# Kernel optimization log

Hardware: AMD Instinct MI355X
Metric: run time of the kernel (lower is better)

Reference implementation:

```python
import jax, jax.numpy as jnp
import numpy as np

D_MODEL = 1024
NUM_HEADS = 16
HEAD_DIM = D_MODEL // NUM_HEADS  # 64
# NOTE: the original module passes scale=attention_head_size, so scores are
# MULTIPLIED by head_dim (64), not divided by sqrt(head_dim). Faithful quirk.
SCALE = float(HEAD_DIM)


def setup_inputs() -> dict:
    key = jax.random.key(0)
    ks = jax.random.split(key, 6)
    bs, s, d = 2, 2048, D_MODEL
    q = jax.random.normal(ks[0], (bs, s, d), dtype=jnp.float32)
    k = jax.random.normal(ks[1], (bs, s, d), dtype=jnp.float32)
    v = jax.random.normal(ks[2], (bs, s, d), dtype=jnp.float32)
    # nn.Linear weights, shape (out, in); no bias (qkv_bias=False)
    init = 1.0 / np.sqrt(d)
    Wq = jax.random.uniform(ks[3], (d, d), jnp.float32, -init, init)
    Wk = jax.random.uniform(ks[4], (d, d), jnp.float32, -init, init)
    Wv = jax.random.uniform(ks[5], (d, d), jnp.float32, -init, init)
    return {"q": q, "k": k, "v": v, "Wq": Wq, "Wk": Wk, "Wv": Wv}


def _split_heads(x):
    bs, s, _ = x.shape
    return x.reshape(bs, s, NUM_HEADS, HEAD_DIM).transpose(0, 2, 1, 3)  # bhsd


def reference(q, k, v, Wq, Wk, Wv):
    bs, s, d = q.shape
    qh = _split_heads(q @ Wq.T)  # [b,h,s,hd]
    kh = _split_heads(k @ Wk.T)
    vh = _split_heads(v @ Wv.T)
    sims = jnp.einsum('bhqd,bhkd->bhqk', qh, kh) * SCALE
    attn = jax.nn.softmax(sims, axis=-1)
    out = jnp.einsum('bhqk,bhkd->bhqd', attn, vh)  # [b,h,s,hd]
    out = out.transpose(0, 2, 1, 3).reshape(bs, s, d)
    return out
```

## Files before the change

### kernel.cpp

```cpp
#include <hip/hip_runtime.h>


typedef _Float16 half4 __attribute__((ext_vector_type(4)));
typedef _Float16 half8 __attribute__((ext_vector_type(8)));
typedef float floatx4 __attribute__((ext_vector_type(4)));

#define MFMA_F16(a, b, c) __builtin_amdgcn_mfma_f32_16x16x32_f16((a), (b), (c), 0, 0, 0)

constexpr int SEQ = 2048;
constexpr int DM = 1024;
constexpr int NH = 16;
constexpr int HD = 64;
constexpr float QSCALE = 92.33248261689366f;

__device__ __forceinline__ void gl2lds16(const _Float16* g, _Float16* l) {
  __builtin_amdgcn_global_load_lds(
      (const __attribute__((address_space(1))) void*)g,
      (__attribute__((address_space(3))) void*)l, 16, 0, 0);
}

__device__ inline void split4(const float4 f, half4& h, half4& l) {
  h[0] = (_Float16)f.x; l[0] = (_Float16)(f.x - (float)h[0]);
  h[1] = (_Float16)f.y; l[1] = (_Float16)(f.y - (float)h[1]);
  h[2] = (_Float16)f.z; l[2] = (_Float16)(f.z - (float)h[2]);
  h[3] = (_Float16)f.w; l[3] = (_Float16)(f.w - (float)h[3]);
}

__global__ __launch_bounds__(256) void convert_kernel(
    const float* __restrict__ x, const float* __restrict__ W,
    _Float16* __restrict__ xh, _Float16* __restrict__ xl,
    _Float16* __restrict__ Wh, _Float16* __restrict__ Wl, int do_lo)
{
  if (blockIdx.x < 4096) {
    int idx = blockIdx.x * 256 + threadIdx.x;
    float4 f = ((const float4*)x)[idx];
    half4 h, l; split4(f, h, l);
    *(half4*)(xh + (size_t)idx * 4) = h;
    if (do_lo) *(half4*)(xl + (size_t)idx * 4) = l;
  } else {
    int idx = (blockIdx.x - 4096) * 256 + threadIdx.x;
    float4 f = ((const float4*)W)[idx];
    half4 h, l; split4(f, h, l);
    *(half4*)(Wh + (size_t)idx * 4) = h;
    if (do_lo) *(half4*)(Wl + (size_t)idx * 4) = l;
  }
}

__global__ __launch_bounds__(256, 1) void proj_kernel(
    const _Float16* __restrict__ Ahg, const _Float16* __restrict__ Alg,
    const _Float16* __restrict__ Bhg, const _Float16* __restrict__ Blg,
    _Float16* __restrict__ yh, _Float16* __restrict__ yl,
    float scale, int three)
{
  __shared__ __align__(16) _Float16 Ahs[128][64];
  __shared__ __align__(16) _Float16 Als[128][64];
  __shared__ __align__(16) _Float16 Bhs[128][64];
  __shared__ __align__(16) _Float16 Bls[128][64];

  const int tid = threadIdx.x;
  const int bm = blockIdx.x;
  const int bn = blockIdx.y;
  const int lane = tid & 63, l15 = lane & 15, quad = lane >> 4;
  const int w = tid >> 6, wm = w >> 1, wn = w & 1;

  const int r8 = lane >> 3;
  const int cp8 = (((lane & 7) ^ r8)) * 8;
  int grow[4]; _Float16* la[4]; _Float16* lal[4]; _Float16* lb[4]; _Float16* lbl[4];
  #pragma unroll
  for (int i = 0; i < 4; i++) {
    const int g = w * 4 + i;
    grow[i] = g * 8 + r8;
    la[i]  = &Ahs[0][0] + g * 512;
    lal[i] = &Als[0][0] + g * 512;
    lb[i]  = &Bhs[0][0] + g * 512;
    lbl[i] = &Bls[0][0] + g * 512;
  }

  floatx4 acc[4][4];
  #pragma unroll
  for (int mt = 0; mt < 4; mt++)
    #pragma unroll
    for (int nt = 0; nt < 4; nt++)
      acc[mt][nt] = (floatx4){0.f, 0.f, 0.f, 0.f};

  for (int kk = 0; kk < DM; kk += 64) {
    __syncthreads();
    #pragma unroll
    for (int i = 0; i < 4; i++) {
      const size_t ga = (size_t)(bm * 128 + grow[i]) * DM + kk + cp8;
      const size_t gb = (size_t)(bn * 128 + grow[i]) * DM + kk + cp8;
      gl2lds16(Ahg + ga, la[i]);
      gl2lds16(Bhg + gb, lb[i]);
      if (three) {
        gl2lds16(Alg + ga, lal[i]);
        gl2lds16(Blg + gb, lbl[i]);
      }
    }
    __syncthreads();

    #pragma unroll
    for (int kc = 0; kc < 2; kc++) {
      const int swz = ((kc * 4 + quad) ^ (l15 & 7)) * 8;
      half8 ah[4], bh_[4], al[4], bl[4];
      #pragma unroll
      for (int t = 0; t < 4; t++) {
        ah[t]  = *(const half8*)&Ahs[wm * 64 + t * 16 + l15][swz];
        bh_[t] = *(const half8*)&Bhs[wn * 64 + t * 16 + l15][swz];
        if (three) {
          al[t] = *(const half8*)&Als[wm * 64 + t * 16 + l15][swz];
          bl[t] = *(const half8*)&Bls[wn * 64 + t * 16 + l15][swz];
        }
      }
      if (three) {
        #pragma unroll
        for (int mt = 0; mt < 4; mt++)
          #pragma unroll
          for (int nt = 0; nt < 4; nt++) {
            floatx4 t0 = MFMA_F16(ah[mt], bh_[nt], acc[mt][nt]);
            t0 = MFMA_F16(ah[mt], bl[nt], t0);
            acc[mt][nt] = MFMA_F16(al[mt], bh_[nt], t0);
          }
      } else {
        #pragma unroll
        for (int mt = 0; mt < 4; mt++)
          #pragma unroll
          for (int nt = 0; nt < 4; nt++)
            acc[mt][nt] = MFMA_F16(ah[mt], bh_[nt], acc[mt][nt]);
      }
    }
  }

  #pragma unroll
  for (int mt = 0; mt < 4; mt++)
    #pragma unroll
    for (int nt = 0; nt < 4; nt++)
      #pragma unroll
      for (int r = 0; r < 4; r++) {
        int gm = bm * 128 + wm * 64 + mt * 16 + quad * 4 + r;
        int gn = bn * 128 + wn * 64 + nt * 16 + l15;
        int b = gm >> 11, s = gm & 2047;
        int h = gn >> 6, d = gn & 63;
        size_t idx = ((size_t)(b * NH + h) * SEQ + s) * HD + d;
        float val = acc[mt][nt][r] * scale;
        _Float16 hi = (_Float16)val;
        yh[idx] = hi;
        if (three) yl[idx] = (_Float16)(val - (float)hi);
      }
}

__global__ __launch_bounds__(256) void transpose_v(const _Float16* __restrict__ vh,
                                                   _Float16* __restrict__ vhT)
{
  __shared__ __align__(16) _Float16 T[128][72];
  const int bh = blockIdx.x, sc = blockIdx.y, tid = threadIdx.x;
  const _Float16* src = vh + ((size_t)bh * SEQ + sc * 128) * HD;
  #pragma unroll
  for (int i = 0; i < 4; i++) {
    int c = i * 256 + tid, row = c >> 3, off = (c & 7) * 8;
    *(half8*)&T[row][off] = *(const half8*)(src + (size_t)row * HD + off);
  }
  __syncthreads();
  _Float16* dst = vhT + (size_t)bh * HD * SEQ + sc * 128;
  #pragma unroll
  for (int i = 0; i < 4; i++) {
    int c = i * 256 + tid, hd = c >> 4, off = (c & 15) * 8;
    int base32 = off & ~31, qsel = (off >> 3) & 3;
    half8 vv;
    #pragma unroll
    for (int j = 0; j < 8; j++) {
      int s_local = base32 + 16 * (j >> 2) + 4 * qsel + (j & 3);
      vv[j] = T[s_local][hd];
    }
    *(half8*)(dst + (size_t)hd * SEQ + off) = vv;
  }
}

__global__ __launch_bounds__(256, 4) void flash_kernel(
    const _Float16* __restrict__ qh_hi, const _Float16* __restrict__ qh_lo,
    const _Float16* __restrict__ kh_hi, const _Float16* __restrict__ kh_lo,
    const _Float16* __restrict__ vhT, float* __restrict__ Op, float2* __restrict__ ml)
{
  __shared__ __align__(16) _Float16 Kh[64][64];
  __shared__ __align__(16) _Float16 Kl[64][64];
  __shared__ __align__(16) _Float16 Vt[64][64];

  const int id = blockIdx.x;
  const int seq_ = id >> 3;
  const int bh = (id & 7) + 8 * (seq_ & 3);
  const int rem = seq_ >> 2;
  const int qb = rem & 15;
  const int kh = rem >> 4;
  const int tid = threadIdx.x;
  const int wq = tid >> 6;
  const int lane = tid & 63, l15 = lane & 15, quad = lane >> 4;

  const size_t bh_off = (size_t)bh * SEQ * HD;
  const _Float16* __restrict__ kh_p = kh_hi + bh_off;
  const _Float16* __restrict__ kl_p = kh_lo + bh_off;
  const _Float16* __restrict__ vt_p = vhT + (size_t)bh * HD * SEQ;
  const int qrow0 = qb * 128 + wq * 32;

  half8 bqh[2][2], bql[2][2];
  #pragma unroll
  for (int g = 0; g < 2; g++) {
    const _Float16* qp_h = qh_hi + bh_off + (size_t)(qrow0 + g * 16 + l15) * HD;
    const _Float16* qp_l = qh_lo + bh_off + (size_t)(qrow0 + g * 16 + l15) * HD;
    #pragma unroll
    for (int kc = 0; kc < 2; kc++) {
      bqh[g][kc] = *(const half8*)(qp_h + kc * 32 + quad * 8);
      bql[g][kc] = *(const half8*)(qp_l + kc * 32 + quad * 8);
    }
  }

  const int r8 = lane >> 3;
  const int cp8 = ((lane & 7) ^ r8) * 8;

  float m_[2] = {-3.0e38f, -3.0e38f};
  float l_[2] = {0.f, 0.f};
  floatx4 Oacc[2][4];
  #pragma unroll
  for (int g = 0; g < 2; g++)
    #pragma unroll
    for (int nd = 0; nd < 4; nd++) Oacc[g][nd] = (floatx4){0.f, 0.f, 0.f, 0.f};

  const int kt0 = kh * 16;
  for (int kt = kt0; kt < kt0 + 16; kt++) {
    const int kbase = kt * 64;
    __syncthreads();
    #pragma unroll
    for (int i = 0; i < 2; i++) {
      const int g = wq * 2 + i;
      const int r = g * 8 + r8;
      gl2lds16(kh_p + (size_t)(kbase + r) * HD + cp8, &Kh[0][0] + g * 512);
      gl2lds16(kl_p + (size_t)(kbase + r) * HD + cp8, &Kl[0][0] + g * 512);
      gl2lds16(vt_p + (size_t)r * SEQ + kbase + cp8, &Vt[0][0] + g * 512);
    }
    __syncthreads();

    floatx4 sacc[2][4];
    #pragma unroll
    for (int nt = 0; nt < 4; nt++) {
      const int r7 = l15 & 7;
      half8 akh0 = *(const half8*)&Kh[nt * 16 + l15][((0 * 4 + quad) ^ r7) * 8];
      half8 akh1 = *(const half8*)&Kh[nt * 16 + l15][((1 * 4 + quad) ^ r7) * 8];
      half8 akl0 = *(const half8*)&Kl[nt * 16 + l15][((0 * 4 + quad) ^ r7) * 8];
      half8 akl1 = *(const half8*)&Kl[nt * 16 + l15][((1 * 4 + quad) ^ r7) * 8];
      #pragma unroll
      for (int g = 0; g < 2; g++) {
        floatx4 s4 = (floatx4){0.f, 0.f, 0.f, 0.f};
        s4 = MFMA_F16(akh0, bqh[g][0], s4);
        s4 = MFMA_F16(akh1, bqh[g][1], s4);
        s4 = MFMA_F16(akh0, bql[g][0], s4);
        s4 = MFMA_F16(akh1, bql[g][1], s4);
        s4 = MFMA_F16(akl0, bqh[g][0], s4);
        s4 = MFMA_F16(akl1, bqh[g][1], s4);
        sacc[g][nt] = s4;
      }
    }

    half8 av[4][2];
    {
      const int r7 = l15 & 7;
      #pragma unroll
      for (int nd = 0; nd < 4; nd++) {
        av[nd][0] = *(const half8*)&Vt[nd * 16 + l15][((0 * 4 + quad) ^ r7) * 8];
        av[nd][1] = *(const half8*)&Vt[nd * 16 + l15][((1 * 4 + quad) ^ r7) * 8];
      }
    }

    #pragma unroll
    for (int g = 0; g < 2; g++) {
      float rmax = sacc[g][0][0];
      #pragma unroll
      for (int nt = 0; nt < 4; nt++)
        #pragma unroll
        for (int r = 0; r < 4; r++) rmax = fmaxf(rmax, sacc[g][nt][r]);
      rmax = fmaxf(rmax, __shfl_xor(rmax, 16, 64));
      rmax = fmaxf(rmax, __shfl_xor(rmax, 32, 64));
      const float mnew = fmaxf(m_[g], rmax);
      const float alpha = exp2f(m_[g] - mnew);
      m_[g] = mnew;

      float rsum = 0.f;
      #pragma unroll
      for (int nt = 0; nt < 4; nt++)
        #pragma unroll
        for (int r = 0; r < 4; r++) {
          float p = exp2f(sacc[g][nt][r] - mnew);
          sacc[g][nt][r] = p;
          rsum += p;
        }
      rsum += __shfl_xor(rsum, 16, 64);
      rsum += __shfl_xor(rsum, 32, 64);
      l_[g] = l_[g] * alpha + rsum;

      half8 bp8[2];
      #pragma unroll
      for (int kc = 0; kc < 2; kc++)
        #pragma unroll
        for (int j = 0; j < 8; j++)
          bp8[kc][j] = (_Float16)sacc[g][2 * kc + (j >> 2)][j & 3];

      #pragma unroll
      for (int nd = 0; nd < 4; nd++) {
        Oacc[g][nd][0] *= alpha; Oacc[g][nd][1] *= alpha;
        Oacc[g][nd][2] *= alpha; Oacc[g][nd][3] *= alpha;
        Oacc[g][nd] = MFMA_F16(av[nd][0], bp8[0], Oacc[g][nd]);
        Oacc[g][nd] = MFMA_F16(av[nd][1], bp8[1], Oacc[g][nd]);
      }
    }
  }

  const size_t fqbase = (size_t)bh * SEQ + qrow0;
  #pragma unroll
  for (int g = 0; g < 2; g++) {
    const size_t fq = fqbase + g * 16 + l15;
    float* ob = Op + ((size_t)kh * 65536 + fq) * HD;
    #pragma unroll
    for (int nd = 0; nd < 4; nd++) {
      float4 vv;
      vv.x = Oacc[g][nd][0]; vv.y = Oacc[g][nd][1];
      vv.z = Oacc[g][nd][2]; vv.w = Oacc[g][nd][3];
      *(float4*)(ob + nd * 16 + quad * 4) = vv;
    }
    if (quad == 0) ml[kh * 65536 + fq] = make_float2(m_[g], l_[g]);
  }
}

__global__ __launch_bounds__(256) void merge_kernel(const float* __restrict__ Op,
                                                    const float2* __restrict__ ml,
                                                    float* __restrict__ out)
{
  const int tid = threadIdx.x;
  const int fq = blockIdx.x * 64 + (tid >> 2);
  const int dp = (tid & 3) * 16;
  float2 m0 = ml[fq], m1 = ml[65536 + fq];
  float M = fmaxf(m0.x, m1.x);
  float w0 = exp2f(m0.x - M), w1 = exp2f(m1.x - M);
  float rinv = 1.0f / (m0.y * w0 + m1.y * w1);
  int bh = fq >> 11, s = fq & 2047, b = bh >> 4, h = bh & 15;
  float* ob = out + ((size_t)(b * SEQ + s)) * DM + h * HD + dp;
  const float* p0 = Op + (size_t)fq * HD + dp;
  const float* p1 = p0 + (size_t)65536 * HD;
  #pragma unroll
  for (int j = 0; j < 4; j++) {
    float4 a = *(const float4*)(p0 + 4 * j);
    float4 c = *(const float4*)(p1 + 4 * j);
    float4 r;
    r.x = (a.x * w0 + c.x * w1) * rinv;
    r.y = (a.y * w0 + c.y * w1) * rinv;
    r.z = (a.z * w0 + c.z * w1) * rinv;
    r.w = (a.w * w0 + c.w * w1) * rinv;
    *(float4*)(ob + 4 * j) = r;
  }
}

extern "C" void kernel_launch(void* const* d_in, const int* in_sizes, int n_in,
                              void* d_out, int out_size, void* d_ws, size_t ws_size,
                              hipStream_t stream) {
  const float* q  = (const float*)d_in[0];
  const float* k  = (const float*)d_in[1];
  const float* v  = (const float*)d_in[2];
  const float* Wq = (const float*)d_in[3];
  const float* Wk = (const float*)d_in[4];
  const float* Wv = (const float*)d_in[5];
  float* out = (float*)d_out;

  char* W = (char*)d_ws;
  const size_t MiB = 1ull << 20;
  _Float16* qh_hi = (_Float16*)(W + 0 * MiB);
  _Float16* qh_lo = (_Float16*)(W + 8 * MiB);
  _Float16* kh_hi = (_Float16*)(W + 16 * MiB);
  _Float16* kh_lo = (_Float16*)(W + 24 * MiB);
  _Float16* vhT   = (_Float16*)(W + 32 * MiB);
  _Float16* vh    = (_Float16*)(W + 40 * MiB);
  _Float16* xh    = (_Float16*)(W + 48 * MiB);
  _Float16* xl    = (_Float16*)(W + 56 * MiB);
  _Float16* Wh    = (_Float16*)(W + 64 * MiB);
  _Float16* Wl    = (_Float16*)(W + 66 * MiB);
  float*    Op    = (float*)  (W + 40 * MiB);
  float2*   mlp   = (float2*) (W + 72 * MiB);

  convert_kernel<<<5120, 256, 0, stream>>>(q, Wq, xh, xl, Wh, Wl, 1);
  proj_kernel<<<dim3(32, 8), 256, 0, stream>>>(xh, xl, Wh, Wl, qh_hi, qh_lo, QSCALE, 1);
  convert_kernel<<<5120, 256, 0, stream>>>(k, Wk, xh, xl, Wh, Wl, 1);
  proj_kernel<<<dim3(32, 8), 256, 0, stream>>>(xh, xl, Wh, Wl, kh_hi, kh_lo, 1.0f, 1);
  convert_kernel<<<5120, 256, 0, stream>>>(v, Wv, xh, xl, Wh, Wl, 0);
  proj_kernel<<<dim3(32, 8), 256, 0, stream>>>(xh, xl, Wh, Wl, vh, vh, 1.0f, 0);

  transpose_v<<<dim3(32, 16), 256, 0, stream>>>(vh, vhT);
  flash_kernel<<<1024, 256, 0, stream>>>(qh_hi, qh_lo, kh_hi, kh_lo, vhT, Op, mlp);
  merge_kernel<<<1024, 256, 0, stream>>>(Op, mlp, out);
}
```

Baseline: 319.7 us.

## Shrink projection M-tile to 64 and register-prefetch next K/V tile in flash kernel

The projection GEMM tile shrinks from 128x128 to 64x128, doubling the grid to 512 blocks and allowing two blocks per CU. The aim is better occupancy and load balance across the GPU's many CUs. The flash kernel now loads the next K/V tile from global memory into registers while computing on the current tile, then writes it to LDS after a barrier, overlapping memory latency with compute. This costs extra registers and an extra barrier per iteration. The projection change also adds B-tile reloads per output element.

```diff
diff --git a/kernel.cpp b/kernel.cpp
--- a/kernel.cpp
+++ b/kernel.cpp
@@ -46,14 +46,14 @@
   }
 }
 
-__global__ __launch_bounds__(256, 1) void proj_kernel(
+__global__ __launch_bounds__(256, 2) void proj_kernel(
     const _Float16* __restrict__ Ahg, const _Float16* __restrict__ Alg,
     const _Float16* __restrict__ Bhg, const _Float16* __restrict__ Blg,
     _Float16* __restrict__ yh, _Float16* __restrict__ yl,
     float scale, int three)
 {
-  __shared__ __align__(16) _Float16 Ahs[128][64];
-  __shared__ __align__(16) _Float16 Als[128][64];
+  __shared__ __align__(16) _Float16 Ahs[64][64];
+  __shared__ __align__(16) _Float16 Als[64][64];
   __shared__ __align__(16) _Float16 Bhs[128][64];
   __shared__ __align__(16) _Float16 Bls[128][64];
 
@@ -64,21 +64,11 @@
   const int w = tid >> 6, wm = w >> 1, wn = w & 1;
 
   const int r8 = lane >> 3;
-  const int cp8 = (((lane & 7) ^ r8)) * 8;
-  int grow[4]; _Float16* la[4]; _Float16* lal[4]; _Float16* lb[4]; _Float16* lbl[4];
-  #pragma unroll
-  for (int i = 0; i < 4; i++) {
-    const int g = w * 4 + i;
-    grow[i] = g * 8 + r8;
-    la[i]  = &Ahs[0][0] + g * 512;
-    lal[i] = &Als[0][0] + g * 512;
-    lb[i]  = &Bhs[0][0] + g * 512;
-    lbl[i] = &Bls[0][0] + g * 512;
-  }
-
-  floatx4 acc[4][4];
-  #pragma unroll
-  for (int mt = 0; mt < 4; mt++)
+  const int cp8 = ((lane & 7) ^ r8) * 8;
+
+  floatx4 acc[2][4];
+  #pragma unroll
+  for (int mt = 0; mt < 2; mt++)
     #pragma unroll
     for (int nt = 0; nt < 4; nt++)
       acc[mt][nt] = (floatx4){0.f, 0.f, 0.f, 0.f};
@@ -86,34 +76,38 @@
   for (int kk = 0; kk < DM; kk += 64) {
     __syncthreads();
     #pragma unroll
+    for (int i = 0; i < 2; i++) {
+      const int g = w * 2 + i;
+      const size_t ga = (size_t)(bm * 64 + g * 8 + r8) * DM + kk + cp8;
+      gl2lds16(Ahg + ga, &Ahs[0][0] + g * 512);
+      if (three) gl2lds16(Alg + ga, &Als[0][0] + g * 512);
+    }
+    #pragma unroll
     for (int i = 0; i < 4; i++) {
-      const size_t ga = (size_t)(bm * 128 + grow[i]) * DM + kk + cp8;
-      const size_t gb = (size_t)(bn * 128 + grow[i]) * DM + kk + cp8;
-      gl2lds16(Ahg + ga, la[i]);
-      gl2lds16(Bhg + gb, lb[i]);
-      if (three) {
-        gl2lds16(Alg + ga, lal[i]);
-        gl2lds16(Blg + gb, lbl[i]);
-      }
+      const int g = w * 4 + i;
+      const size_t gb = (size_t)(bn * 128 + g * 8 + r8) * DM + kk + cp8;
+      gl2lds16(Bhg + gb, &Bhs[0][0] + g * 512);
+      if (three) gl2lds16(Blg + gb, &Bls[0][0] + g * 512);
     }
     __syncthreads();
 
     #pragma unroll
     for (int kc = 0; kc < 2; kc++) {
       const int swz = ((kc * 4 + quad) ^ (l15 & 7)) * 8;
-      half8 ah[4], bh_[4], al[4], bl[4];
-      #pragma unroll
-      for (int t = 0; t < 4; t++) {
-        ah[t]  = *(const half8*)&Ahs[wm * 64 + t * 16 + l15][swz];
-        bh_[t] = *(const half8*)&Bhs[wn * 64 + t * 16 + l15][swz];
-        if (three) {
-          al[t] = *(const half8*)&Als[wm * 64 + t * 16 + l15][swz];
-          bl[t] = *(const half8*)&Bls[wn * 64 + t * 16 + l15][swz];
-        }
+      half8 ah[2], al[2], bh_[4], bl[4];
+      #pragma unroll
+      for (int mt = 0; mt < 2; mt++) {
+        ah[mt] = *(const half8*)&Ahs[wm * 32 + mt * 16 + l15][swz];
+        if (three) al[mt] = *(const half8*)&Als[wm * 32 + mt * 16 + l15][swz];
+      }
+      #pragma unroll
+      for (int nt = 0; nt < 4; nt++) {
+        bh_[nt] = *(const half8*)&Bhs[wn * 64 + nt * 16 + l15][swz];
+        if (three) bl[nt] = *(const half8*)&Bls[wn * 64 + nt * 16 + l15][swz];
       }
       if (three) {
         #pragma unroll
-        for (int mt = 0; mt < 4; mt++)
+        for (int mt = 0; mt < 2; mt++)
           #pragma unroll
           for (int nt = 0; nt < 4; nt++) {
             floatx4 t0 = MFMA_F16(ah[mt], bh_[nt], acc[mt][nt]);
@@ -122,7 +116,7 @@
           }
       } else {
         #pragma unroll
-        for (int mt = 0; mt < 4; mt++)
+        for (int mt = 0; mt < 2; mt++)
           #pragma unroll
           for (int nt = 0; nt < 4; nt++)
             acc[mt][nt] = MFMA_F16(ah[mt], bh_[nt], acc[mt][nt]);
@@ -131,12 +125,12 @@
   }
 
   #pragma unroll
-  for (int mt = 0; mt < 4; mt++)
+  for (int mt = 0; mt < 2; mt++)
     #pragma unroll
     for (int nt = 0; nt < 4; nt++)
       #pragma unroll
       for (int r = 0; r < 4; r++) {
-        int gm = bm * 128 + wm * 64 + mt * 16 + quad * 4 + r;
+        int gm = bm * 64 + wm * 32 + mt * 16 + quad * 4 + r;
         int gn = bn * 128 + wn * 64 + nt * 16 + l15;
         int b = gm >> 11, s = gm & 2047;
         int h = gn >> 6, d = gn & 63;
@@ -224,9 +218,8 @@
     for (int nd = 0; nd < 4; nd++) Oacc[g][nd] = (floatx4){0.f, 0.f, 0.f, 0.f};
 
   const int kt0 = kh * 16;
-  for (int kt = kt0; kt < kt0 + 16; kt++) {
-    const int kbase = kt * 64;
-    __syncthreads();
+  {
+    const int kbase = kt0 * 64;
     #pragma unroll
     for (int i = 0; i < 2; i++) {
       const int g = wq * 2 + i;
@@ -235,7 +228,24 @@
       gl2lds16(kl_p + (size_t)(kbase + r) * HD + cp8, &Kl[0][0] + g * 512);
       gl2lds16(vt_p + (size_t)r * SEQ + kbase + cp8, &Vt[0][0] + g * 512);
     }
+  }
+
+  for (int kt = kt0; kt < kt0 + 16; kt++) {
     __syncthreads();
+
+    const bool hasnext = (kt + 1 < kt0 + 16);
+    half8 rkh[2], rkl[2], rvt[2];
+    if (hasnext) {
+      const int kb2 = (kt + 1) * 64;
+      #pragma unroll
+      for (int i = 0; i < 2; i++) {
+        const int g = wq * 2 + i;
+        const int r = g * 8 + r8;
+        rkh[i] = *(const half8*)(kh_p + (size_t)(kb2 + r) * HD + cp8);
+        rkl[i] = *(const half8*)(kl_p + (size_t)(kb2 + r) * HD + cp8);
+        rvt[i] = *(const half8*)(vt_p + (size_t)r * SEQ + kb2 + cp8);
+      }
+    }
 
     floatx4 sacc[2][4];
     #pragma unroll
@@ -307,6 +317,17 @@
         Oacc[g][nd][2] *= alpha; Oacc[g][nd][3] *= alpha;
         Oacc[g][nd] = MFMA_F16(av[nd][0], bp8[0], Oacc[g][nd]);
         Oacc[g][nd] = MFMA_F16(av[nd][1], bp8[1], Oacc[g][nd]);
+      }
+    }
+
+    __syncthreads();
+    if (hasnext) {
+      #pragma unroll
+      for (int i = 0; i < 2; i++) {
+        const int g = wq * 2 + i;
+        *(half8*)(&Kh[0][0] + g * 512 + lane * 8) = rkh[i];
+        *(half8*)(&Kl[0][0] + g * 512 + lane * 8) = rkl[i];
+        *(half8*)(&Vt[0][0] + g * 512 + lane * 8) = rvt[i];
       }
     }
   }
@@ -382,11 +403,11 @@
   float2*   mlp   = (float2*) (W + 72 * MiB);
 
   convert_kernel<<<5120, 256, 0, stream>>>(q, Wq, xh, xl, Wh, Wl, 1);
-  proj_kernel<<<dim3(32, 8), 256, 0, stream>>>(xh, xl, Wh, Wl, qh_hi, qh_lo, QSCALE, 1);
+  proj_kernel<<<dim3(64, 8), 256, 0, stream>>>(xh, xl, Wh, Wl, qh_hi, qh_lo, QSCALE, 1);
   convert_kernel<<<5120, 256, 0, stream>>>(k, Wk, xh, xl, Wh, Wl, 1);
-  proj_kernel<<<dim3(32, 8), 256, 0, stream>>>(xh, xl, Wh, Wl, kh_hi, kh_lo, 1.0f, 1);
+  proj_kernel<<<dim3(64, 8), 256, 0, stream>>>(xh, xl, Wh, Wl, kh_hi, kh_lo, 1.0f, 1);
   convert_kernel<<<5120, 256, 0, stream>>>(v, Wv, xh, xl, Wh, Wl, 0);
-  proj_kernel<<<dim3(32, 8), 256, 0, stream>>>(xh, xl, Wh, Wl, vh, vh, 1.0f, 0);
+  proj_kernel<<<dim3(64, 8), 256, 0, stream>>>(xh, xl, Wh, Wl, vh, vh, 1.0f, 0);
 
   transpose_v<<<dim3(32, 16), 256, 0, stream>>>(vh, vhT);
   flash_kernel<<<1024, 256, 0, stream>>>(qh_hi, qh_lo, kh_hi, kh_lo, vhT, Op, mlp);
```

New measurement: 518.6 us. 62.2% more time.

## Split KV range four ways and load V fragments directly from global

Applied to the files above, without the earlier changes.

The flash kernel is templated on the number of KV splits. When the workspace allows, it launches 2048 blocks with a 4-way KV split and a matching generalized merge kernel, which doubles grid parallelism. V tiles no longer go through LDS; each lane reads its half8 V fragments straight from the pre-transposed global buffer, which removes one LDS buffer and its async copies. The tradeoff is more partial-output traffic in the merge and uncoalesced, uncached-in-LDS global V reads. The block-index decoding also changes, which may break whichever bh/qb mapping the previous ordering intended.

```diff
diff --git a/kernel.cpp b/kernel.cpp
--- a/kernel.cpp
+++ b/kernel.cpp
@@ -175,6 +175,7 @@
   }
 }
 
+template<int KSPLIT>
 __global__ __launch_bounds__(256, 4) void flash_kernel(
     const _Float16* __restrict__ qh_hi, const _Float16* __restrict__ qh_lo,
     const _Float16* __restrict__ kh_hi, const _Float16* __restrict__ kh_lo,
@@ -182,12 +183,11 @@
 {
   __shared__ __align__(16) _Float16 Kh[64][64];
   __shared__ __align__(16) _Float16 Kl[64][64];
-  __shared__ __align__(16) _Float16 Vt[64][64];
-
+
+  constexpr int NKT = 32 / KSPLIT;
   const int id = blockIdx.x;
-  const int seq_ = id >> 3;
-  const int bh = (id & 7) + 8 * (seq_ & 3);
-  const int rem = seq_ >> 2;
+  const int bh = (id & 7) + 8 * ((id >> 3) & 3);
+  const int rem = id >> 5;
   const int qb = rem & 15;
   const int kh = rem >> 4;
   const int tid = threadIdx.x;
@@ -223,8 +223,8 @@
     #pragma unroll
     for (int nd = 0; nd < 4; nd++) Oacc[g][nd] = (floatx4){0.f, 0.f, 0.f, 0.f};
 
-  const int kt0 = kh * 16;
-  for (int kt = kt0; kt < kt0 + 16; kt++) {
+  const int kt0 = kh * NKT;
+  for (int kt = kt0; kt < kt0 + NKT; kt++) {
     const int kbase = kt * 64;
     __syncthreads();
     #pragma unroll
@@ -233,7 +233,6 @@
       const int r = g * 8 + r8;
       gl2lds16(kh_p + (size_t)(kbase + r) * HD + cp8, &Kh[0][0] + g * 512);
       gl2lds16(kl_p + (size_t)(kbase + r) * HD + cp8, &Kl[0][0] + g * 512);
-      gl2lds16(vt_p + (size_t)r * SEQ + kbase + cp8, &Vt[0][0] + g * 512);
     }
     __syncthreads();
 
@@ -259,13 +258,11 @@
     }
 
     half8 av[4][2];
-    {
-      const int r7 = l15 & 7;
-      #pragma unroll
-      for (int nd = 0; nd < 4; nd++) {
-        av[nd][0] = *(const half8*)&Vt[nd * 16 + l15][((0 * 4 + quad) ^ r7) * 8];
-        av[nd][1] = *(const half8*)&Vt[nd * 16 + l15][((1 * 4 + quad) ^ r7) * 8];
-      }
+    #pragma unroll
+    for (int nd = 0; nd < 4; nd++) {
+      const _Float16* vp = vt_p + (size_t)(nd * 16 + l15) * SEQ + kbase;
+      av[nd][0] = *(const half8*)(vp + quad * 8);
+      av[nd][1] = *(const half8*)(vp + 32 + quad * 8);
     }
 
     #pragma unroll
@@ -327,6 +324,7 @@
   }
 }
 
+template<int KSPLIT>
 __global__ __launch_bounds__(256) void merge_kernel(const float* __restrict__ Op,
                                                     const float2* __restrict__ ml,
                                                     float* __restrict__ out)
@@ -334,23 +332,33 @@
   const int tid = threadIdx.x;
   const int fq = blockIdx.x * 64 + (tid >> 2);
   const int dp = (tid & 3) * 16;
-  float2 m0 = ml[fq], m1 = ml[65536 + fq];
-  float M = fmaxf(m0.x, m1.x);
-  float w0 = exp2f(m0.x - M), w1 = exp2f(m1.x - M);
-  float rinv = 1.0f / (m0.y * w0 + m1.y * w1);
-  int bh = fq >> 11, s = fq & 2047, b = bh >> 4, h = bh & 15;
-  float* ob = out + ((size_t)(b * SEQ + s)) * DM + h * HD + dp;
+  float2 mls[KSPLIT];
+  float M = -3.0e38f;
+  #pragma unroll
+  for (int s = 0; s < KSPLIT; s++) {
+    mls[s] = ml[s * 65536 + fq];
+    M = fmaxf(M, mls[s].x);
+  }
+  float wsum = 0.f, w[KSPLIT];
+  #pragma unroll
+  for (int s = 0; s < KSPLIT; s++) {
+    w[s] = exp2f(mls[s].x - M);
+    wsum += mls[s].y * w[s];
+  }
+  const float rinv = 1.0f / wsum;
+  int bh = fq >> 11, sq = fq & 2047, b = bh >> 4, h = bh & 15;
+  float* ob = out + ((size_t)(b * SEQ + sq)) * DM + h * HD + dp;
   const float* p0 = Op + (size_t)fq * HD + dp;
-  const float* p1 = p0 + (size_t)65536 * HD;
   #pragma unroll
   for (int j = 0; j < 4; j++) {
-    float4 a = *(const float4*)(p0 + 4 * j);
-    float4 c = *(const float4*)(p1 + 4 * j);
-    float4 r;
-    r.x = (a.x * w0 + c.x * w1) * rinv;
-    r.y = (a.y * w0 + c.y * w1) * rinv;
-    r.z = (a.z * w0 + c.z * w1) * rinv;
-    r.w = (a.w * w0 + c.w * w1) * rinv;
+    float4 r = make_float4(0.f, 0.f, 0.f, 0.f);
+    #pragma unroll
+    for (int s = 0; s < KSPLIT; s++) {
+      float4 a = *(const float4*)(p0 + (size_t)s * 65536 * HD + 4 * j);
+      r.x += a.x * w[s]; r.y += a.y * w[s];
+      r.z += a.z * w[s]; r.w += a.w * w[s];
+    }
+    r.x *= rinv; r.y *= rinv; r.z *= rinv; r.w *= rinv;
     *(float4*)(ob + 4 * j) = r;
   }
 }
@@ -379,7 +387,6 @@
   _Float16* Wh    = (_Float16*)(W + 64 * MiB);
   _Float16* Wl    = (_Float16*)(W + 66 * MiB);
   float*    Op    = (float*)  (W + 40 * MiB);
-  float2*   mlp   = (float2*) (W + 72 * MiB);
 
   convert_kernel<<<5120, 256, 0, stream>>>(q, Wq, xh, xl, Wh, Wl, 1);
   proj_kernel<<<dim3(32, 8), 256, 0, stream>>>(xh, xl, Wh, Wl, qh_hi, qh_lo, QSCALE, 1);
@@ -389,6 +396,14 @@
   proj_kernel<<<dim3(32, 8), 256, 0, stream>>>(xh, xl, Wh, Wl, vh, vh, 1.0f, 0);
 
   transpose_v<<<dim3(32, 16), 256, 0, stream>>>(vh, vhT);
-  flash_kernel<<<1024, 256, 0, stream>>>(qh_hi, qh_lo, kh_hi, kh_lo, vhT, Op, mlp);
-  merge_kernel<<<1024, 256, 0, stream>>>(Op, mlp, out);
-}
+
+  if (ws_size == 0 || ws_size >= 106 * MiB) {
+    float2* mlp = (float2*)(W + 104 * MiB);
+    flash_kernel<4><<<2048, 256, 0, stream>>>(qh_hi, qh_lo, kh_hi, kh_lo, vhT, Op, mlp);
+    merge_kernel<4><<<1024, 256, 0, stream>>>(Op, mlp, out);
+  } else {
+    float2* mlp = (float2*)(W + 72 * MiB);
+    flash_kernel<2><<<1024, 256, 0, stream>>>(qh_hi, qh_lo, kh_hi, kh_lo, vhT, Op, mlp);
+    merge_kernel<2><<<1024, 256, 0, stream>>>(Op, mlp, out);
+  }
+}
```

Result: slower. 382.3 us (+19.6%).

## Double-buffer LDS tiles to prefetch next K-slice in projection and flash kernels

Applied to the files above, without the earlier changes.

The projection GEMM now keeps two LDS buffers for the A/B hi/lo tiles. It issues the global-to-LDS loads for the next 64-wide K slice before computing on the current one, which removes one barrier per iteration. The flash kernel double-buffers the K hi/lo tiles and prefetches the next key block, and it loads V into a single buffer that it reads only after a mid-iteration barrier. The aim is to hide global load latency behind MFMA work. In exchange, LDS use grows (flash to 40KB per block, projection to 128KB), which may limit occupancy. The mid-loop barrier in the flash kernel also waits on the prefetch, so the overlap there is only partial.

```diff
diff --git a/kernel.cpp b/kernel.cpp
--- a/kernel.cpp
+++ b/kernel.cpp
@@ -52,10 +52,10 @@
     _Float16* __restrict__ yh, _Float16* __restrict__ yl,
     float scale, int three)
 {
-  __shared__ __align__(16) _Float16 Ahs[128][64];
-  __shared__ __align__(16) _Float16 Als[128][64];
-  __shared__ __align__(16) _Float16 Bhs[128][64];
-  __shared__ __align__(16) _Float16 Bls[128][64];
+  __shared__ __align__(16) _Float16 Ahs[2][128][64];
+  __shared__ __align__(16) _Float16 Als[2][128][64];
+  __shared__ __align__(16) _Float16 Bhs[2][128][64];
+  __shared__ __align__(16) _Float16 Bls[2][128][64];
 
   const int tid = threadIdx.x;
   const int bm = blockIdx.x;
@@ -65,50 +65,60 @@
 
   const int r8 = lane >> 3;
   const int cp8 = (((lane & 7) ^ r8)) * 8;
-  int grow[4]; _Float16* la[4]; _Float16* lal[4]; _Float16* lb[4]; _Float16* lbl[4];
+  int grow[4];
+  #pragma unroll
+  for (int i = 0; i < 4; i++) grow[i] = (w * 4 + i) * 8 + r8;
+
+  floatx4 acc[4][4];
+  #pragma unroll
+  for (int mt = 0; mt < 4; mt++)
+    #pragma unroll
+    for (int nt = 0; nt < 4; nt++)
+      acc[mt][nt] = (floatx4){0.f, 0.f, 0.f, 0.f};
+
   #pragma unroll
   for (int i = 0; i < 4; i++) {
     const int g = w * 4 + i;
-    grow[i] = g * 8 + r8;
-    la[i]  = &Ahs[0][0] + g * 512;
-    lal[i] = &Als[0][0] + g * 512;
-    lb[i]  = &Bhs[0][0] + g * 512;
-    lbl[i] = &Bls[0][0] + g * 512;
-  }
-
-  floatx4 acc[4][4];
-  #pragma unroll
-  for (int mt = 0; mt < 4; mt++)
-    #pragma unroll
-    for (int nt = 0; nt < 4; nt++)
-      acc[mt][nt] = (floatx4){0.f, 0.f, 0.f, 0.f};
-
-  for (int kk = 0; kk < DM; kk += 64) {
+    const size_t ga = (size_t)(bm * 128 + grow[i]) * DM + cp8;
+    const size_t gb = (size_t)(bn * 128 + grow[i]) * DM + cp8;
+    gl2lds16(Ahg + ga, &Ahs[0][0][0] + g * 512);
+    gl2lds16(Bhg + gb, &Bhs[0][0][0] + g * 512);
+    if (three) {
+      gl2lds16(Alg + ga, &Als[0][0][0] + g * 512);
+      gl2lds16(Blg + gb, &Bls[0][0][0] + g * 512);
+    }
+  }
+
+  for (int t = 0; t < 16; t++) {
+    const int cur = t & 1;
     __syncthreads();
-    #pragma unroll
-    for (int i = 0; i < 4; i++) {
-      const size_t ga = (size_t)(bm * 128 + grow[i]) * DM + kk + cp8;
-      const size_t gb = (size_t)(bn * 128 + grow[i]) * DM + kk + cp8;
-      gl2lds16(Ahg + ga, la[i]);
-      gl2lds16(Bhg + gb, lb[i]);
-      if (three) {
-        gl2lds16(Alg + ga, lal[i]);
-        gl2lds16(Blg + gb, lbl[i]);
-      }
-    }
-    __syncthreads();
+    if (t + 1 < 16) {
+      const int kk = (t + 1) * 64, nxt = cur ^ 1;
+      #pragma unroll
+      for (int i = 0; i < 4; i++) {
+        const int g = w * 4 + i;
+        const size_t ga = (size_t)(bm * 128 + grow[i]) * DM + kk + cp8;
+        const size_t gb = (size_t)(bn * 128 + grow[i]) * DM + kk + cp8;
+        gl2lds16(Ahg + ga, &Ahs[nxt][0][0] + g * 512);
+        gl2lds16(Bhg + gb, &Bhs[nxt][0][0] + g * 512);
+        if (three) {
+          gl2lds16(Alg + ga, &Als[nxt][0][0] + g * 512);
+          gl2lds16(Blg + gb, &Bls[nxt][0][0] + g * 512);
+        }
+      }
+    }
 
     #pragma unroll
     for (int kc = 0; kc < 2; kc++) {
       const int swz = ((kc * 4 + quad) ^ (l15 & 7)) * 8;
       half8 ah[4], bh_[4], al[4], bl[4];
       #pragma unroll
-      for (int t = 0; t < 4; t++) {
-        ah[t]  = *(const half8*)&Ahs[wm * 64 + t * 16 + l15][swz];
-        bh_[t] = *(const half8*)&Bhs[wn * 64 + t * 16 + l15][swz];
+      for (int tt = 0; tt < 4; tt++) {
+        ah[tt]  = *(const half8*)&Ahs[cur][wm * 64 + tt * 16 + l15][swz];
+        bh_[tt] = *(const half8*)&Bhs[cur][wn * 64 + tt * 16 + l15][swz];
         if (three) {
-          al[t] = *(const half8*)&Als[wm * 64 + t * 16 + l15][swz];
-          bl[t] = *(const half8*)&Bls[wn * 64 + t * 16 + l15][swz];
+          al[tt] = *(const half8*)&Als[cur][wm * 64 + tt * 16 + l15][swz];
+          bl[tt] = *(const half8*)&Bls[cur][wn * 64 + tt * 16 + l15][swz];
         }
       }
       if (three) {
@@ -180,8 +190,8 @@
     const _Float16* __restrict__ kh_hi, const _Float16* __restrict__ kh_lo,
     const _Float16* __restrict__ vhT, float* __restrict__ Op, float2* __restrict__ ml)
 {
-  __shared__ __align__(16) _Float16 Kh[64][64];
-  __shared__ __align__(16) _Float16 Kl[64][64];
+  __shared__ __align__(16) _Float16 Kh[2][64][64];
+  __shared__ __align__(16) _Float16 Kl[2][64][64];
   __shared__ __align__(16) _Float16 Vt[64][64];
 
   const int id = blockIdx.x;
@@ -224,27 +234,47 @@
     for (int nd = 0; nd < 4; nd++) Oacc[g][nd] = (floatx4){0.f, 0.f, 0.f, 0.f};
 
   const int kt0 = kh * 16;
-  for (int kt = kt0; kt < kt0 + 16; kt++) {
-    const int kbase = kt * 64;
-    __syncthreads();
+  {
+    const int kbase = kt0 * 64;
     #pragma unroll
     for (int i = 0; i < 2; i++) {
       const int g = wq * 2 + i;
       const int r = g * 8 + r8;
-      gl2lds16(kh_p + (size_t)(kbase + r) * HD + cp8, &Kh[0][0] + g * 512);
-      gl2lds16(kl_p + (size_t)(kbase + r) * HD + cp8, &Kl[0][0] + g * 512);
+      gl2lds16(kh_p + (size_t)(kbase + r) * HD + cp8, &Kh[0][0][0] + g * 512);
+      gl2lds16(kl_p + (size_t)(kbase + r) * HD + cp8, &Kl[0][0][0] + g * 512);
+    }
+  }
+
+  for (int kt = kt0; kt < kt0 + 16; kt++) {
+    const int cur = kt & 1;
+    const int kbase = kt * 64;
+    __syncthreads();
+
+    #pragma unroll
+    for (int i = 0; i < 2; i++) {
+      const int g = wq * 2 + i;
+      const int r = g * 8 + r8;
       gl2lds16(vt_p + (size_t)r * SEQ + kbase + cp8, &Vt[0][0] + g * 512);
     }
-    __syncthreads();
+    if (kt + 1 < kt0 + 16) {
+      const int kb2 = (kt + 1) * 64, nxt = cur ^ 1;
+      #pragma unroll
+      for (int i = 0; i < 2; i++) {
+        const int g = wq * 2 + i;
+        const int r = g * 8 + r8;
+        gl2lds16(kh_p + (size_t)(kb2 + r) * HD + cp8, &Kh[nxt][0][0] + g * 512);
+        gl2lds16(kl_p + (size_t)(kb2 + r) * HD + cp8, &Kl[nxt][0][0] + g * 512);
+      }
+    }
 
     floatx4 sacc[2][4];
+    const int r7 = l15 & 7;
     #pragma unroll
     for (int nt = 0; nt < 4; nt++) {
-      const int r7 = l15 & 7;
-      half8 akh0 = *(const half8*)&Kh[nt * 16 + l15][((0 * 4 + quad) ^ r7) * 8];
-      half8 akh1 = *(const half8*)&Kh[nt * 16 + l15][((1 * 4 + quad) ^ r7) * 8];
-      half8 akl0 = *(const half8*)&Kl[nt * 16 + l15][((0 * 4 + quad) ^ r7) * 8];
-      half8 akl1 = *(const half8*)&Kl[nt * 16 + l15][((1 * 4 + quad) ^ r7) * 8];
+      half8 akh0 = *(const half8*)&Kh[cur][nt * 16 + l15][((0 * 4 + quad) ^ r7) * 8];
+      half8 akh1 = *(const half8*)&Kh[cur][nt * 16 + l15][((1 * 4 + quad) ^ r7) * 8];
+      half8 akl0 = *(const half8*)&Kl[cur][nt * 16 + l15][((0 * 4 + quad) ^ r7) * 8];
+      half8 akl1 = *(const half8*)&Kl[cur][nt * 16 + l15][((1 * 4 + quad) ^ r7) * 8];
       #pragma unroll
       for (int g = 0; g < 2; g++) {
         floatx4 s4 = (floatx4){0.f, 0.f, 0.f, 0.f};
@@ -258,16 +288,8 @@
       }
     }
 
-    half8 av[4][2];
-    {
-      const int r7 = l15 & 7;
-      #pragma unroll
-      for (int nd = 0; nd < 4; nd++) {
-        av[nd][0] = *(const half8*)&Vt[nd * 16 + l15][((0 * 4 + quad) ^ r7) * 8];
-        av[nd][1] = *(const half8*)&Vt[nd * 16 + l15][((1 * 4 + quad) ^ r7) * 8];
-      }
-    }
-
+    float alpha2[2];
+    half8 bp8g[2][2];
     #pragma unroll
     for (int g = 0; g < 2; g++) {
       float rmax = sacc[g][0][0];
@@ -278,7 +300,7 @@
       rmax = fmaxf(rmax, __shfl_xor(rmax, 16, 64));
       rmax = fmaxf(rmax, __shfl_xor(rmax, 32, 64));
       const float mnew = fmaxf(m_[g], rmax);
-      const float alpha = exp2f(m_[g] - mnew);
+      alpha2[g] = exp2f(m_[g] - mnew);
       m_[g] = mnew;
 
       float rsum = 0.f;
@@ -292,21 +314,32 @@
         }
       rsum += __shfl_xor(rsum, 16, 64);
       rsum += __shfl_xor(rsum, 32, 64);
-      l_[g] = l_[g] * alpha + rsum;
-
-      half8 bp8[2];
+      l_[g] = l_[g] * alpha2[g] + rsum;
+
       #pragma unroll
       for (int kc = 0; kc < 2; kc++)
         #pragma unroll
         for (int j = 0; j < 8; j++)
-          bp8[kc][j] = (_Float16)sacc[g][2 * kc + (j >> 2)][j & 3];
-
+          bp8g[g][kc][j] = (_Float16)sacc[g][2 * kc + (j >> 2)][j & 3];
+    }
+
+    __syncthreads();
+
+    half8 av[4][2];
+    #pragma unroll
+    for (int nd = 0; nd < 4; nd++) {
+      av[nd][0] = *(const half8*)&Vt[nd * 16 + l15][((0 * 4 + quad) ^ r7) * 8];
+      av[nd][1] = *(const half8*)&Vt[nd * 16 + l15][((1 * 4 + quad) ^ r7) * 8];
+    }
+
+    #pragma unroll
+    for (int g = 0; g < 2; g++) {
       #pragma unroll
       for (int nd = 0; nd < 4; nd++) {
-        Oacc[g][nd][0] *= alpha; Oacc[g][nd][1] *= alpha;
-        Oacc[g][nd][2] *= alpha; Oacc[g][nd][3] *= alpha;
-        Oacc[g][nd] = MFMA_F16(av[nd][0], bp8[0], Oacc[g][nd]);
-        Oacc[g][nd] = MFMA_F16(av[nd][1], bp8[1], Oacc[g][nd]);
+        Oacc[g][nd][0] *= alpha2[g]; Oacc[g][nd][1] *= alpha2[g];
+        Oacc[g][nd][2] *= alpha2[g]; Oacc[g][nd][3] *= alpha2[g];
+        Oacc[g][nd] = MFMA_F16(av[nd][0], bp8g[g][0], Oacc[g][nd]);
+        Oacc[g][nd] = MFMA_F16(av[nd][1], bp8g[g][1], Oacc[g][nd]);
       }
     }
   }
```

Result: no change. 322.0 us (+0.7%).
